# Performance work log

Hardware: AMD Instinct MI355X
Metric: run time of the kernel (lower is better)

The kernel has to match this reference:

```python
import jax, jax.numpy as jnp
import numpy as np

N = 100000   # nodes
E = 3200000  # edges (avg degree 32)
G = 64       # graphs in batch
K = 4        # TAGConv hops
H = 16       # hidden_size
F = 2        # num_node_features
SLOPE = 0.01 # LeakyReLU default negative slope


def setup_inputs():
    key = jax.random.key(0)
    ks = jax.random.split(key, 10)
    s = 0.1
    return {
        "x": jax.random.normal(ks[0], (N, F), jnp.float32),
        "edge_index": jax.random.randint(ks[1], (2, E), 0, N),
        "edge_attr": jax.random.uniform(ks[2], (E, 7), jnp.float32),
        "batch": jnp.sort(jax.random.randint(ks[3], (N,), 0, G)),
        # conv1: K+1 hop weights [K+1, F, H] + bias [H]
        "W1": jax.random.normal(ks[4], (K + 1, F, H), jnp.float32) * s,
        "b1": jax.random.normal(ks[5], (H,), jnp.float32) * s,
        # 2 more TAGConv layers: [2, K+1, H, H] + [2, H]
        "Wl": jax.random.normal(ks[6], (2, K + 1, H, H), jnp.float32) * s,
        "bl": jax.random.normal(ks[7], (2, H), jnp.float32) * s,
        # singleLinear (reghead_layers == 1): [H, 1] + [1]
        "Ws": jax.random.normal(ks[8], (H, 1), jnp.float32) * s,
        "bs": jax.random.normal(ks[9], (1,), jnp.float32) * s,
    }


def _leaky(v):
    return jnp.where(v >= 0, v, SLOPE * v)


def _tag_conv(x, src, dst, norm, W, b):
    # out = sum_k (A_hat^k x) @ W[k] + b   (PyG TAGConv, normalize=True)
    out = x @ W[0]
    h = x
    for k in range(1, W.shape[0]):
        # gather from source, weight by normalized edge weight, scatter-add to dest
        h = jax.ops.segment_sum(h[src] * norm[:, None], dst, num_segments=x.shape[0])
        out = out + h @ W[k]
    return out + b


def reference(x, edge_index, edge_attr, batch, W1, b1, Wl, bl, Ws, bs):
    src, dst = edge_index[0], edge_index[1]
    w = edge_attr[:, 6]
    # gcn_norm without self-loops: D^{-1/2} A D^{-1/2}
    deg = jax.ops.segment_sum(w, dst, num_segments=x.shape[0])
    dinv = jnp.where(deg > 0, jax.lax.rsqrt(jnp.where(deg > 0, deg, 1.0)), 0.0)
    norm = dinv[src] * w * dinv[dst]

    h = _leaky(_tag_conv(x, src, dst, norm, W1, b1))      # dropout is eval-mode identity
    for i in range(Wl.shape[0]):
        h = _leaky(_tag_conv(h, src, dst, norm, Wl[i], bl[i]))

    # global_mean_pool over graph ids
    counts = jax.ops.segment_sum(jnp.ones((x.shape[0],), h.dtype), batch, num_segments=G)
    pooled = jax.ops.segment_sum(h, batch, num_segments=G) / jnp.maximum(counts, 1.0)[:, None]

    return pooled @ Ws + bs  # [G, 1]
```

## Files before the change

### kernel.cpp

```cpp
#include <hip/hip_runtime.h>
#include <hip/hip_fp16.h>

#define SLOPE 0.01f
#define CAP 80u

__device__ __forceinline__ float leaky(float v){ return v >= 0.f ? v : SLOPE * v; }
__device__ __forceinline__ unsigned short h2u(float f){ return __half_as_ushort(__float2half(f)); }
__device__ __forceinline__ float u2f(unsigned short u){ return __half2float(__ushort_as_half(u)); }

__global__ __launch_bounds__(256) void k_build(const int* __restrict__ src, const int* __restrict__ dst,
                                               const float* __restrict__ attr,
                                               unsigned long long* __restrict__ packed,
                                               uint2* __restrict__ fat, int E){
    int e = blockIdx.x * 256 + threadIdx.x;
    if (e >= E) return;
    float w = attr[(size_t)e * 7 + 6];
    int d = dst[e];
    int s = src[e];
    unsigned long long add = (1ull << 40) | (unsigned long long)(w * 16777216.0f);
    unsigned long long old = atomicAdd(&packed[d], add);
    unsigned rank = (unsigned)(old >> 40);
    if (rank < CAP){
        uint2 r; r.x = (unsigned)s; r.y = __float_as_uint(w);
        fat[(size_t)d * CAP + rank] = r;
    }
}

__global__ __launch_bounds__(256) void k_dinv_bsum(const unsigned long long* __restrict__ packed,
                                                   float* __restrict__ dinv, unsigned* __restrict__ cnt,
                                                   unsigned* __restrict__ bsum, int n){
    int gid = blockIdx.x * 256 + threadIdx.x;
    unsigned c = 0;
    if (gid < n){
        unsigned long long p = packed[gid];
        float deg = (float)(p & ((1ull << 40) - 1)) * (1.0f / 16777216.0f);
        dinv[gid] = deg > 0.f ? rsqrtf(deg) : 0.f;
        c = min((unsigned)(p >> 40), CAP);
        cnt[gid] = c;
    }
    unsigned v = c;
    #pragma unroll
    for (int off = 32; off; off >>= 1) v += __shfl_down(v, off);
    __shared__ unsigned s[4];
    int lane = threadIdx.x & 63, wid = threadIdx.x >> 6;
    if (lane == 0) s[wid] = v;
    __syncthreads();
    if (threadIdx.x == 0) bsum[blockIdx.x] = s[0] + s[1] + s[2] + s[3];
}

__global__ __launch_bounds__(1024) void k_scanb(unsigned* __restrict__ bsum, unsigned* __restrict__ total_out, int nb){
    int t = threadIdx.x;
    int lane = t & 63, wid = t >> 6;
    unsigned v = t < nb ? bsum[t] : 0u;
    unsigned inc = v;
    #pragma unroll
    for (int off = 1; off < 64; off <<= 1){
        unsigned u = __shfl_up(inc, off);
        if (lane >= off) inc += u;
    }
    __shared__ unsigned sw[16];
    if (lane == 63) sw[wid] = inc;
    __syncthreads();
    if (wid == 0 && lane < 16){
        unsigned w = sw[lane];
        #pragma unroll
        for (int off = 1; off < 16; off <<= 1){
            unsigned u = __shfl_up(w, off, 16);
            if (lane >= off) w += u;
        }
        sw[lane] = w;
    }
    __syncthreads();
    unsigned waveoff = wid ? sw[wid - 1] : 0u;
    unsigned excl = waveoff + inc - v;
    if (t < nb) bsum[t] = excl;
    if (t == nb - 1) *total_out = excl + v;
}

__global__ __launch_bounds__(256) void k_scanfinal(const unsigned* __restrict__ cnt, const unsigned* __restrict__ bsum,
                                                   unsigned* __restrict__ rowptr, int n){
    int gid = blockIdx.x * 256 + threadIdx.x;
    unsigned v = gid < n ? cnt[gid] : 0u;
    int lane = threadIdx.x & 63, wid = threadIdx.x >> 6;
    unsigned inc = v;
    #pragma unroll
    for (int off = 1; off < 64; off <<= 1){
        unsigned u = __shfl_up(inc, off);
        if (lane >= off) inc += u;
    }
    __shared__ unsigned sw[4];
    if (lane == 63) sw[wid] = inc;
    __syncthreads();
    unsigned woff = 0;
    for (int i = 0; i < wid; i++) woff += sw[i];
    unsigned excl = bsum[blockIdx.x] + woff + inc - v;
    if (gid < n) rowptr[gid] = excl;
}

__global__ __launch_bounds__(256) void k_compact(const uint2* __restrict__ fat, const unsigned* __restrict__ cnt,
                                                 const unsigned* __restrict__ rowptr, const float* __restrict__ dinv,
                                                 unsigned* __restrict__ csrc, __half* __restrict__ cnrm, int n){
    int gt = blockIdx.x * 256 + threadIdx.x;
    int node = gt >> 4, k0 = gt & 15;
    if (node >= n) return;
    unsigned c = cnt[node], base = rowptr[node];
    float dv = dinv[node];
    const uint2* row = fat + (size_t)node * CAP;
    for (unsigned k = k0; k < c; k += 16){
        uint2 r = row[k];
        float nrm = dinv[r.x] * __uint_as_float(r.y) * dv;
        csrc[base + k] = r.x;
        cnrm[base + k] = __float2half(nrm);
    }
}

__global__ __launch_bounds__(256) void k_prop2_first(const float2* __restrict__ x, const unsigned* __restrict__ rowptr,
                                                     const unsigned* __restrict__ csrc, const __half* __restrict__ cnrm,
                                                     const float* __restrict__ W1, const float* __restrict__ b1,
                                                     __half2* __restrict__ hout, __half* __restrict__ outAcc, int n){
    __shared__ float sW[64], sb[16];
    int t = threadIdx.x;
    if (t < 64) sW[t] = W1[t];
    if (t < 16) sb[t] = b1[t];
    __syncthreads();
    int gt = blockIdx.x * 256 + t;
    int node = gt >> 4, f = gt & 15;
    if (node >= n) return;
    unsigned beg = rowptr[node], end = rowptr[node + 1];
    float a0 = 0.f, a1 = 0.f;
    for (unsigned i = beg + (unsigned)f; i < end; i += 16){
        float nrm = __half2float(cnrm[i]);
        float2 h = x[csrc[i]];
        a0 = fmaf(nrm, h.x, a0);
        a1 = fmaf(nrm, h.y, a1);
    }
    #pragma unroll
    for (int m = 1; m < 16; m <<= 1){
        a0 += __shfl_xor(a0, m, 64);
        a1 += __shfl_xor(a1, m, 64);
    }
    if (f == 0){
        __half2 hh; hh.x = __float2half(a0); hh.y = __float2half(a1);
        hout[node] = hh;
    }
    float2 xo = x[node];
    float val = sb[f] + xo.x * sW[f] + xo.y * sW[16 + f] + a0 * sW[32 + f] + a1 * sW[48 + f];
    outAcc[(size_t)node * 16 + f] = __float2half(val);
}

__global__ __launch_bounds__(256) void k_prop2_mid(const __half2* __restrict__ hin, const unsigned* __restrict__ rowptr,
                                                   const unsigned* __restrict__ csrc, const __half* __restrict__ cnrm,
                                                   const float* __restrict__ Wk,
                                                   __half2* __restrict__ hout, __half* __restrict__ outAcc, int n){
    __shared__ float sW[32];
    int t = threadIdx.x;
    if (t < 32) sW[t] = Wk[t];
    __syncthreads();
    int gt = blockIdx.x * 256 + t;
    int node = gt >> 4, f = gt & 15;
    if (node >= n) return;
    unsigned beg = rowptr[node], end = rowptr[node + 1];
    float a0 = 0.f, a1 = 0.f;
    for (unsigned i = beg + (unsigned)f; i < end; i += 16){
        float nrm = __half2float(cnrm[i]);
        __half2 h = hin[csrc[i]];
        a0 = fmaf(nrm, __low2float(h), a0);
        a1 = fmaf(nrm, __high2float(h), a1);
    }
    #pragma unroll
    for (int m = 1; m < 16; m <<= 1){
        a0 += __shfl_xor(a0, m, 64);
        a1 += __shfl_xor(a1, m, 64);
    }
    if (f == 0){
        __half2 hh; hh.x = __float2half(a0); hh.y = __float2half(a1);
        hout[node] = hh;
    }
    size_t oi = (size_t)node * 16 + f;
    float val = __half2float(outAcc[oi]) + a0 * sW[f] + a1 * sW[16 + f];
    outAcc[oi] = __float2half(val);
}

__global__ __launch_bounds__(256) void k_prop2_last(const __half2* __restrict__ hin, const unsigned* __restrict__ rowptr,
                                                    const unsigned* __restrict__ csrc, const __half* __restrict__ cnrm,
                                                    const float* __restrict__ Wk,
                                                    const float* __restrict__ W0n, const float* __restrict__ bn,
                                                    __half* __restrict__ outAcc, __half* __restrict__ hNext, int n){
    __shared__ float sWk[32], sW0[256], sb[16];
    int t = threadIdx.x;
    if (t < 32) sWk[t] = Wk[t];
    sW0[t] = W0n[t];
    if (t < 16) sb[t] = bn[t];
    __syncthreads();
    int gt = blockIdx.x * 256 + t;
    int node = gt >> 4, f = gt & 15;
    if (node >= n) return;
    unsigned beg = rowptr[node], end = rowptr[node + 1];
    float a0 = 0.f, a1 = 0.f;
    for (unsigned i = beg + (unsigned)f; i < end; i += 16){
        float nrm = __half2float(cnrm[i]);
        __half2 h = hin[csrc[i]];
        a0 = fmaf(nrm, __low2float(h), a0);
        a1 = fmaf(nrm, __high2float(h), a1);
    }
    #pragma unroll
    for (int m = 1; m < 16; m <<= 1){
        a0 += __shfl_xor(a0, m, 64);
        a1 += __shfl_xor(a1, m, 64);
    }
    size_t oi = (size_t)node * 16 + f;
    float val = __half2float(outAcc[oi]) + a0 * sWk[f] + a1 * sWk[16 + f];
    float hv = leaky(val);
    hNext[oi] = __float2half(hv);
    int base = (t & 63) & 48;
    float o2 = sb[f];
    #pragma unroll
    for (int fp = 0; fp < 16; fp++){
        float u = __shfl(hv, base + fp, 64);
        o2 = fmaf(u, sW0[fp * 16 + f], o2);
    }
    outAcc[oi] = __float2half(o2);
}

template<int MODE>
__global__ __launch_bounds__(256) void k_prop16(const __half* __restrict__ hin, const unsigned* __restrict__ rowptr,
                                                const unsigned* __restrict__ csrc, const __half* __restrict__ cnrm,
                                                const float* __restrict__ Wk,
                                                __half* __restrict__ hout, __half* __restrict__ outAcc,
                                                __half* __restrict__ hNext,
                                                const float* __restrict__ W0n, const float* __restrict__ bn, int n){
    __shared__ float sW[256], sW2[256], sb[16];
    int t = threadIdx.x;
    sW[t] = Wk[t];
    if (MODE == 1){
        sW2[t] = W0n[t];
        if (t < 16) sb[t] = bn[t];
    }
    __syncthreads();
    int gt = blockIdx.x * 256 + t;
    int node = gt >> 4, f = gt & 15;
    if (node >= n) return;
    unsigned beg = rowptr[node], end = rowptr[node + 1];
    int base = (t & 63) & 48;
    float acc = 0.f;
    for (unsigned kb = beg; kb < end; kb += 16){
        unsigned idx = kb + (unsigned)f;
        unsigned sreg = 0; float nreg = 0.f;
        if (idx < end){
            sreg = csrc[idx];
            nreg = __half2float(cnrm[idx]);
        }
        unsigned m = min(16u, end - kb);
        for (unsigned k = 0; k < m; k++){
            unsigned s = (unsigned)__shfl((int)sreg, base + (int)k, 64);
            float nm = __shfl(nreg, base + (int)k, 64);
            acc = fmaf(nm, __half2float(hin[(size_t)s * 16 + f]), acc);
        }
    }
    if (MODE == 0) hout[(size_t)node * 16 + f] = __float2half(acc);
    float o = 0.f;
    #pragma unroll
    for (int fp = 0; fp < 16; fp++){
        float v = __shfl(acc, base + fp, 64);
        o = fmaf(v, sW[fp * 16 + f], o);
    }
    size_t oi = (size_t)node * 16 + f;
    if (MODE == 0){
        float v = __half2float(outAcc[oi]) + o;
        outAcc[oi] = __float2half(v);
    } else {
        float v = __half2float(outAcc[oi]) + o;
        float hv = leaky(v);
        hNext[oi] = __float2half(hv);
        if (MODE == 1){
            float o2 = sb[f];
            #pragma unroll
            for (int fp = 0; fp < 16; fp++){
                float u = __shfl(hv, base + fp, 64);
                o2 = fmaf(u, sW2[fp * 16 + f], o2);
            }
            outAcc[oi] = __float2half(o2);
        }
    }
}

__global__ __launch_bounds__(256) void k_pool(const __half* __restrict__ h, const int* __restrict__ batch,
                                              const float* __restrict__ Ws, const float* __restrict__ bs,
                                              float* __restrict__ out, int n){
    int g = blockIdx.x;
    int lo = 0, hi = n;
    while (lo < hi){ int mid = (lo + hi) >> 1; if (batch[mid] < g) lo = mid + 1; else hi = mid; }
    int start = lo;
    lo = start; hi = n;
    while (lo < hi){ int mid = (lo + hi) >> 1; if (batch[mid] < g + 1) lo = mid + 1; else hi = mid; }
    int end = lo;
    int t = threadIdx.x;
    int slot = t >> 4, f = t & 15;
    float acc = 0.f;
    for (int node = start + slot; node < end; node += 16)
        acc += __half2float(h[(size_t)node * 16 + f]);
    __shared__ float red[256];
    red[t] = acc;
    __syncthreads();
    if (t < 16){
        float s = 0.f;
        for (int sl = 0; sl < 16; sl++) s += red[sl * 16 + t];
        float cntf = (float)max(end - start, 1);
        red[t] = (s / cntf) * Ws[t];
    }
    __syncthreads();
    if (t == 0){
        float r = bs[0];
        for (int i = 0; i < 16; i++) r += red[i];
        out[g] = r;
    }
}

extern "C" void kernel_launch(void* const* d_in, const int* in_sizes, int n_in,
                              void* d_out, int out_size, void* d_ws, size_t ws_size,
                              hipStream_t stream){
    const float* x    = (const float*)d_in[0];
    const int*   ei   = (const int*)d_in[1];
    const float* attr = (const float*)d_in[2];
    const int*   batch= (const int*)d_in[3];
    const float* W1   = (const float*)d_in[4];
    const float* b1   = (const float*)d_in[5];
    const float* Wl   = (const float*)d_in[6];
    const float* bl   = (const float*)d_in[7];
    const float* Ws   = (const float*)d_in[8];
    const float* bs   = (const float*)d_in[9];
    float* out = (float*)d_out;

    const int N = in_sizes[0] / 2;
    const int E = in_sizes[1] / 2;
    const int* src = ei;
    const int* dst = ei + E;

    char* ws = (char*)d_ws;
    size_t off = 0;
    auto alloc = [&](size_t bytes){ void* p = ws + off; off += (bytes + 255) & ~(size_t)255; return p; };
    uint2*    fat    = (uint2*)   alloc((size_t)N * CAP * 8);
    unsigned* csrc   = (unsigned*)alloc((size_t)E * 4);
    __half*   cnrm   = (__half*)  alloc((size_t)E * 2);
    unsigned long long* packed = (unsigned long long*)alloc((size_t)N * 8);
    float*    dinv   = (float*)   alloc((size_t)N * 4);
    unsigned* rowptr = (unsigned*)alloc((size_t)(N + 1) * 4);
    unsigned* cnt    = (unsigned*)alloc((size_t)N * 4);
    unsigned* bsum   = (unsigned*)alloc((size_t)1024 * 4);
    char* fr = (char*)fat;
    __half*   hA     = (__half*)  fr;                 fr += ((size_t)N * 16 * 2 + 255) & ~(size_t)255;
    __half*   hB     = (__half*)  fr;                 fr += ((size_t)N * 16 * 2 + 255) & ~(size_t)255;
    __half*   outAcc = (__half*)  fr;                 fr += ((size_t)N * 16 * 2 + 255) & ~(size_t)255;
    __half2*  h2a    = (__half2*) fr;                 fr += ((size_t)N * 4 + 255) & ~(size_t)255;
    __half2*  h2b    = (__half2*) fr;

    const int TB = 256;
    const int gE   = (E + TB - 1) / TB;
    const int gN   = (N + TB - 1) / TB;
    const int gN16 = (N * 16 + TB - 1) / TB;
    const int nb   = (N + 255) / 256;

    hipMemsetAsync(packed, 0, (size_t)N * 8, stream);
    k_build    <<<gE, TB, 0, stream>>>(src, dst, attr, packed, fat, E);
    k_dinv_bsum<<<nb, 256, 0, stream>>>(packed, dinv, cnt, bsum, N);
    k_scanb    <<<1, 1024, 0, stream>>>(bsum, rowptr + N, nb);
    k_scanfinal<<<nb, 256, 0, stream>>>(cnt, bsum, rowptr, N);
    k_compact  <<<gN16, TB, 0, stream>>>(fat, cnt, rowptr, dinv, csrc, cnrm, N);

    k_prop2_first<<<gN16, TB, 0, stream>>>((const float2*)x, rowptr, csrc, cnrm, W1, b1, h2a, outAcc, N);
    k_prop2_mid  <<<gN16, TB, 0, stream>>>(h2a, rowptr, csrc, cnrm, W1 + 2 * 32, h2b, outAcc, N);
    k_prop2_mid  <<<gN16, TB, 0, stream>>>(h2b, rowptr, csrc, cnrm, W1 + 3 * 32, h2a, outAcc, N);
    k_prop2_last <<<gN16, TB, 0, stream>>>(h2a, rowptr, csrc, cnrm, W1 + 4 * 32, Wl, bl, outAcc, hA, N);

    k_prop16<0><<<gN16, TB, 0, stream>>>(hA, rowptr, csrc, cnrm, Wl + 1 * 256, hB, outAcc, nullptr, nullptr, nullptr, N);
    k_prop16<0><<<gN16, TB, 0, stream>>>(hB, rowptr, csrc, cnrm, Wl + 2 * 256, hA, outAcc, nullptr, nullptr, nullptr, N);
    k_prop16<0><<<gN16, TB, 0, stream>>>(hA, rowptr, csrc, cnrm, Wl + 3 * 256, hB, outAcc, nullptr, nullptr, nullptr, N);
    k_prop16<1><<<gN16, TB, 0, stream>>>(hB, rowptr, csrc, cnrm, Wl + 4 * 256, nullptr, outAcc, hA,
                                         Wl + 5 * 256, bl + 16, N);

    const float* W3 = Wl + 5 * 256;
    k_prop16<0><<<gN16, TB, 0, stream>>>(hA, rowptr, csrc, cnrm, W3 + 1 * 256, hB, outAcc, nullptr, nullptr, nullptr, N);
    k_prop16<0><<<gN16, TB, 0, stream>>>(hB, rowptr, csrc, cnrm, W3 + 2 * 256, hA, outAcc, nullptr, nullptr, nullptr, N);
    k_prop16<0><<<gN16, TB, 0, stream>>>(hA, rowptr, csrc, cnrm, W3 + 3 * 256, hB, outAcc, nullptr, nullptr, nullptr, N);
    k_prop16<2><<<gN16, TB, 0, stream>>>(hB, rowptr, csrc, cnrm, W3 + 4 * 256, nullptr, outAcc, hA,
                                         nullptr, nullptr, N);

    k_pool<<<64, 256, 0, stream>>>(hA, batch, Ws, bs, out, N);
}
```

Measured before the change: 747.7 us.

## Interleave CSR src/norm into uint2 and remap prop16 to 4 lanes per node

Merges the separate CSR source-index and half-precision norm arrays into one interleaved uint2 array with an fp32 norm, so each edge needs a single 8-byte load. The 16-feature propagation kernel changes from 16 threads per node with scalar half loads to 4 threads per node, each gathering 4 features with one 8-byte vector load and doing vectorized outAcc read-modify-write. This cuts thread count and instruction overhead per gathered row, but doubles CSR storage and edge-metadata traffic and lowers parallelism per node, which may hurt latency hiding on high-degree rows.

```diff
diff --git a/kernel.cpp b/kernel.cpp
--- a/kernel.cpp
+++ b/kernel.cpp
@@ -7,6 +7,9 @@
 __device__ __forceinline__ float leaky(float v){ return v >= 0.f ? v : SLOPE * v; }
 __device__ __forceinline__ unsigned short h2u(float f){ return __half_as_ushort(__float2half(f)); }
 __device__ __forceinline__ float u2f(unsigned short u){ return __half2float(__ushort_as_half(u)); }
+__device__ __forceinline__ unsigned pk2(float a, float b){
+    return (unsigned)h2u(a) | ((unsigned)h2u(b) << 16);
+}
 
 __global__ __launch_bounds__(256) void k_build(const int* __restrict__ src, const int* __restrict__ dst,
                                                const float* __restrict__ attr,
@@ -99,7 +102,7 @@
 
 __global__ __launch_bounds__(256) void k_compact(const uint2* __restrict__ fat, const unsigned* __restrict__ cnt,
                                                  const unsigned* __restrict__ rowptr, const float* __restrict__ dinv,
-                                                 unsigned* __restrict__ csrc, __half* __restrict__ cnrm, int n){
+                                                 uint2* __restrict__ csr, int n){
     int gt = blockIdx.x * 256 + threadIdx.x;
     int node = gt >> 4, k0 = gt & 15;
     if (node >= n) return;
@@ -109,13 +112,13 @@
     for (unsigned k = k0; k < c; k += 16){
         uint2 r = row[k];
         float nrm = dinv[r.x] * __uint_as_float(r.y) * dv;
-        csrc[base + k] = r.x;
-        cnrm[base + k] = __float2half(nrm);
+        r.y = __float_as_uint(nrm);
+        csr[base + k] = r;
     }
 }
 
 __global__ __launch_bounds__(256) void k_prop2_first(const float2* __restrict__ x, const unsigned* __restrict__ rowptr,
-                                                     const unsigned* __restrict__ csrc, const __half* __restrict__ cnrm,
+                                                     const uint2* __restrict__ csr,
                                                      const float* __restrict__ W1, const float* __restrict__ b1,
                                                      __half2* __restrict__ hout, __half* __restrict__ outAcc, int n){
     __shared__ float sW[64], sb[16];
@@ -129,8 +132,9 @@
     unsigned beg = rowptr[node], end = rowptr[node + 1];
     float a0 = 0.f, a1 = 0.f;
     for (unsigned i = beg + (unsigned)f; i < end; i += 16){
-        float nrm = __half2float(cnrm[i]);
-        float2 h = x[csrc[i]];
+        uint2 r = csr[i];
+        float nrm = __uint_as_float(r.y);
+        float2 h = x[r.x];
         a0 = fmaf(nrm, h.x, a0);
         a1 = fmaf(nrm, h.y, a1);
     }
@@ -149,8 +153,7 @@
 }
 
 __global__ __launch_bounds__(256) void k_prop2_mid(const __half2* __restrict__ hin, const unsigned* __restrict__ rowptr,
-                                                   const unsigned* __restrict__ csrc, const __half* __restrict__ cnrm,
-                                                   const float* __restrict__ Wk,
+                                                   const uint2* __restrict__ csr, const float* __restrict__ Wk,
                                                    __half2* __restrict__ hout, __half* __restrict__ outAcc, int n){
     __shared__ float sW[32];
     int t = threadIdx.x;
@@ -162,8 +165,9 @@
     unsigned beg = rowptr[node], end = rowptr[node + 1];
     float a0 = 0.f, a1 = 0.f;
     for (unsigned i = beg + (unsigned)f; i < end; i += 16){
-        float nrm = __half2float(cnrm[i]);
-        __half2 h = hin[csrc[i]];
+        uint2 r = csr[i];
+        float nrm = __uint_as_float(r.y);
+        __half2 h = hin[r.x];
         a0 = fmaf(nrm, __low2float(h), a0);
         a1 = fmaf(nrm, __high2float(h), a1);
     }
@@ -182,8 +186,7 @@
 }
 
 __global__ __launch_bounds__(256) void k_prop2_last(const __half2* __restrict__ hin, const unsigned* __restrict__ rowptr,
-                                                    const unsigned* __restrict__ csrc, const __half* __restrict__ cnrm,
-                                                    const float* __restrict__ Wk,
+                                                    const uint2* __restrict__ csr, const float* __restrict__ Wk,
                                                     const float* __restrict__ W0n, const float* __restrict__ bn,
                                                     __half* __restrict__ outAcc, __half* __restrict__ hNext, int n){
     __shared__ float sWk[32], sW0[256], sb[16];
@@ -198,8 +201,9 @@
     unsigned beg = rowptr[node], end = rowptr[node + 1];
     float a0 = 0.f, a1 = 0.f;
     for (unsigned i = beg + (unsigned)f; i < end; i += 16){
-        float nrm = __half2float(cnrm[i]);
-        __half2 h = hin[csrc[i]];
+        uint2 r = csr[i];
+        float nrm = __uint_as_float(r.y);
+        __half2 h = hin[r.x];
         a0 = fmaf(nrm, __low2float(h), a0);
         a1 = fmaf(nrm, __high2float(h), a1);
     }
@@ -224,8 +228,7 @@
 
 template<int MODE>
 __global__ __launch_bounds__(256) void k_prop16(const __half* __restrict__ hin, const unsigned* __restrict__ rowptr,
-                                                const unsigned* __restrict__ csrc, const __half* __restrict__ cnrm,
-                                                const float* __restrict__ Wk,
+                                                const uint2* __restrict__ csr, const float* __restrict__ Wk,
                                                 __half* __restrict__ hout, __half* __restrict__ outAcc,
                                                 __half* __restrict__ hNext,
                                                 const float* __restrict__ W0n, const float* __restrict__ bn, int n){
@@ -238,48 +241,72 @@
     }
     __syncthreads();
     int gt = blockIdx.x * 256 + t;
-    int node = gt >> 4, f = gt & 15;
+    int node = gt >> 2, g4 = gt & 3;
     if (node >= n) return;
     unsigned beg = rowptr[node], end = rowptr[node + 1];
-    int base = (t & 63) & 48;
-    float acc = 0.f;
-    for (unsigned kb = beg; kb < end; kb += 16){
-        unsigned idx = kb + (unsigned)f;
-        unsigned sreg = 0; float nreg = 0.f;
+    int base = (t & 63) & 60;
+    int f0 = g4 * 4;
+    float acc[4] = {0.f, 0.f, 0.f, 0.f};
+    for (unsigned kb = beg; kb < end; kb += 4){
+        unsigned idx = kb + (unsigned)g4;
+        unsigned sreg = 0u; float nreg = 0.f;
         if (idx < end){
-            sreg = csrc[idx];
-            nreg = __half2float(cnrm[idx]);
+            uint2 r = csr[idx];
+            sreg = r.x; nreg = __uint_as_float(r.y);
         }
-        unsigned m = min(16u, end - kb);
+        unsigned m = min(4u, end - kb);
         for (unsigned k = 0; k < m; k++){
             unsigned s = (unsigned)__shfl((int)sreg, base + (int)k, 64);
             float nm = __shfl(nreg, base + (int)k, 64);
-            acc = fmaf(nm, __half2float(hin[(size_t)s * 16 + f]), acc);
+            uint2 hv = *(const uint2*)(hin + (size_t)s * 16 + f0);
+            acc[0] = fmaf(nm, u2f((unsigned short)hv.x), acc[0]);
+            acc[1] = fmaf(nm, u2f((unsigned short)(hv.x >> 16)), acc[1]);
+            acc[2] = fmaf(nm, u2f((unsigned short)hv.y), acc[2]);
+            acc[3] = fmaf(nm, u2f((unsigned short)(hv.y >> 16)), acc[3]);
         }
     }
-    if (MODE == 0) hout[(size_t)node * 16 + f] = __float2half(acc);
-    float o = 0.f;
-    #pragma unroll
-    for (int fp = 0; fp < 16; fp++){
-        float v = __shfl(acc, base + fp, 64);
-        o = fmaf(v, sW[fp * 16 + f], o);
-    }
-    size_t oi = (size_t)node * 16 + f;
     if (MODE == 0){
-        float v = __half2float(outAcc[oi]) + o;
-        outAcc[oi] = __float2half(v);
+        uint2 hw; hw.x = pk2(acc[0], acc[1]); hw.y = pk2(acc[2], acc[3]);
+        *(uint2*)(hout + (size_t)node * 16 + f0) = hw;
+    }
+    float o[4] = {0.f, 0.f, 0.f, 0.f};
+    #pragma unroll
+    for (int fpg = 0; fpg < 4; fpg++){
+        #pragma unroll
+        for (int j = 0; j < 4; j++){
+            float v = __shfl(acc[j], base + fpg, 64);
+            int fp = fpg * 4 + j;
+            #pragma unroll
+            for (int jj = 0; jj < 4; jj++) o[jj] = fmaf(v, sW[fp * 16 + f0 + jj], o[jj]);
+        }
+    }
+    uint2* oaP = (uint2*)(outAcc + (size_t)node * 16 + f0);
+    uint2 ov = *oaP;
+    float c0 = u2f((unsigned short)ov.x), c1 = u2f((unsigned short)(ov.x >> 16));
+    float c2 = u2f((unsigned short)ov.y), c3 = u2f((unsigned short)(ov.y >> 16));
+    if (MODE == 0){
+        uint2 nv; nv.x = pk2(c0 + o[0], c1 + o[1]); nv.y = pk2(c2 + o[2], c3 + o[3]);
+        *oaP = nv;
     } else {
-        float v = __half2float(outAcc[oi]) + o;
-        float hv = leaky(v);
-        hNext[oi] = __float2half(hv);
+        float hvr[4];
+        hvr[0] = leaky(c0 + o[0]); hvr[1] = leaky(c1 + o[1]);
+        hvr[2] = leaky(c2 + o[2]); hvr[3] = leaky(c3 + o[3]);
+        uint2 hw; hw.x = pk2(hvr[0], hvr[1]); hw.y = pk2(hvr[2], hvr[3]);
+        *(uint2*)(hNext + (size_t)node * 16 + f0) = hw;
         if (MODE == 1){
-            float o2 = sb[f];
+            float o2[4] = {sb[f0], sb[f0 + 1], sb[f0 + 2], sb[f0 + 3]};
             #pragma unroll
-            for (int fp = 0; fp < 16; fp++){
-                float u = __shfl(hv, base + fp, 64);
-                o2 = fmaf(u, sW2[fp * 16 + f], o2);
+            for (int fpg = 0; fpg < 4; fpg++){
+                #pragma unroll
+                for (int j = 0; j < 4; j++){
+                    float u = __shfl(hvr[j], base + fpg, 64);
+                    int fp = fpg * 4 + j;
+                    #pragma unroll
+                    for (int jj = 0; jj < 4; jj++) o2[jj] = fmaf(u, sW2[fp * 16 + f0 + jj], o2[jj]);
+                }
             }
-            outAcc[oi] = __float2half(o2);
+            uint2 nv; nv.x = pk2(o2[0], o2[1]); nv.y = pk2(o2[2], o2[3]);
+            *oaP = nv;
         }
     }
 }
@@ -340,8 +367,7 @@
     size_t off = 0;
     auto alloc = [&](size_t bytes){ void* p = ws + off; off += (bytes + 255) & ~(size_t)255; return p; };
     uint2*    fat    = (uint2*)   alloc((size_t)N * CAP * 8);
-    unsigned* csrc   = (unsigned*)alloc((size_t)E * 4);
-    __half*   cnrm   = (__half*)  alloc((size_t)E * 2);
+    uint2*    csr    = (uint2*)   alloc((size_t)E * 8);
     unsigned long long* packed = (unsigned long long*)alloc((size_t)N * 8);
     float*    dinv   = (float*)   alloc((size_t)N * 4);
     unsigned* rowptr = (unsigned*)alloc((size_t)(N + 1) * 4);
@@ -356,8 +382,8 @@
 
     const int TB = 256;
     const int gE   = (E + TB - 1) / TB;
-    const int gN   = (N + TB - 1) / TB;
     const int gN16 = (N * 16 + TB - 1) / TB;
+    const int gN4  = (N * 4 + TB - 1) / TB;
     const int nb   = (N + 255) / 256;
 
     hipMemsetAsync(packed, 0, (size_t)N * 8, stream);
@@ -365,25 +391,25 @@
     k_dinv_bsum<<<nb, 256, 0, stream>>>(packed, dinv, cnt, bsum, N);
     k_scanb    <<<1, 1024, 0, stream>>>(bsum, rowptr + N, nb);
     k_scanfinal<<<nb, 256, 0, stream>>>(cnt, bsum, rowptr, N);
-    k_compact  <<<gN16, TB, 0, stream>>>(fat, cnt, rowptr, dinv, csrc, cnrm, N);
-
-    k_prop2_first<<<gN16, TB, 0, stream>>>((const float2*)x, rowptr, csrc, cnrm, W1, b1, h2a, outAcc, N);
-    k_prop2_mid  <<<gN16, TB, 0, stream>>>(h2a, rowptr, csrc, cnrm, W1 + 2 * 32, h2b, outAcc, N);
-    k_prop2_mid  <<<gN16, TB, 0, stream>>>(h2b, rowptr, csrc, cnrm, W1 + 3 * 32, h2a, outAcc, N);
-    k_prop2_last <<<gN16, TB, 0, stream>>>(h2a, rowptr, csrc, cnrm, W1 + 4 * 32, Wl, bl, outAcc, hA, N);
-
-    k_prop16<0><<<gN16, TB, 0, stream>>>(hA, rowptr, csrc, cnrm, Wl + 1 * 256, hB, outAcc, nullptr, nullptr, nullptr, N);
-    k_prop16<0><<<gN16, TB, 0, stream>>>(hB, rowptr, csrc, cnrm, Wl + 2 * 256, hA, outAcc, nullptr, nullptr, nullptr, N);
-    k_prop16<0><<<gN16, TB, 0, stream>>>(hA, rowptr, csrc, cnrm, Wl + 3 * 256, hB, outAcc, nullptr, nullptr, nullptr, N);
-    k_prop16<1><<<gN16, TB, 0, stream>>>(hB, rowptr, csrc, cnrm, Wl + 4 * 256, nullptr, outAcc, hA,
-                                         Wl + 5 * 256, bl + 16, N);
+    k_compact  <<<gN16, TB, 0, stream>>>(fat, cnt, rowptr, dinv, csr, N);
+
+    k_prop2_first<<<gN16, TB, 0, stream>>>((const float2*)x, rowptr, csr, W1, b1, h2a, outAcc, N);
+    k_prop2_mid  <<<gN16, TB, 0, stream>>>(h2a, rowptr, csr, W1 + 2 * 32, h2b, outAcc, N);
+    k_prop2_mid  <<<gN16, TB, 0, stream>>>(h2b, rowptr, csr, W1 + 3 * 32, h2a, outAcc, N);
+    k_prop2_last <<<gN16, TB, 0, stream>>>(h2a, rowptr, csr, W1 + 4 * 32, Wl, bl, outAcc, hA, N);
+
+    k_prop16<0><<<gN4, TB, 0, stream>>>(hA, rowptr, csr, Wl + 1 * 256, hB, outAcc, nullptr, nullptr, nullptr, N);
+    k_prop16<0><<<gN4, TB, 0, stream>>>(hB, rowptr, csr, Wl + 2 * 256, hA, outAcc, nullptr, nullptr, nullptr, N);
+    k_prop16<0><<<gN4, TB, 0, stream>>>(hA, rowptr, csr, Wl + 3 * 256, hB, outAcc, nullptr, nullptr, nullptr, N);
+    k_prop16<1><<<gN4, TB, 0, stream>>>(hB, rowptr, csr, Wl + 4 * 256, nullptr, outAcc, hA,
+                                        Wl + 5 * 256, bl + 16, N);
 
     const float* W3 = Wl + 5 * 256;
-    k_prop16<0><<<gN16, TB, 0, stream>>>(hA, rowptr, csrc, cnrm, W3 + 1 * 256, hB, outAcc, nullptr, nullptr, nullptr, N);
-    k_prop16<0><<<gN16, TB, 0, stream>>>(hB, rowptr, csrc, cnrm, W3 + 2 * 256, hA, outAcc, nullptr, nullptr, nullptr, N);
-    k_prop16<0><<<gN16, TB, 0, stream>>>(hA, rowptr, csrc, cnrm, W3 + 3 * 256, hB, outAcc, nullptr, nullptr, nullptr, N);
-    k_prop16<2><<<gN16, TB, 0, stream>>>(hB, rowptr, csrc, cnrm, W3 + 4 * 256, nullptr, outAcc, hA,
-                                         nullptr, nullptr, N);
+    k_prop16<0><<<gN4, TB, 0, stream>>>(hA, rowptr, csr, W3 + 1 * 256, hB, outAcc, nullptr, nullptr, nullptr, N);
+    k_prop16<0><<<gN4, TB, 0, stream>>>(hB, rowptr, csr, W3 + 2 * 256, hA, outAcc, nullptr, nullptr, nullptr, N);
+    k_prop16<0><<<gN4, TB, 0, stream>>>(hA, rowptr, csr, W3 + 3 * 256, hB, outAcc, nullptr, nullptr, nullptr, N);
+    k_prop16<2><<<gN4, TB, 0, stream>>>(hB, rowptr, csr, W3 + 4 * 256, nullptr, outAcc, hA,
+                                        nullptr, nullptr, N);
 
     k_pool<<<64, 256, 0, stream>>>(hA, batch, Ws, bs, out, N);
 }
```

New measurement: 639.4 us. 1.17x faster.
